# Kernel tuning notes

Measured on AMD Instinct MI355X. Metric: run time of the kernel, lower is better.

## Reference

```python
import jax, jax.numpy as jnp
import numpy as np
from math import sqrt, log

N_PATCHES = 128
ATTN_WINDOW = 10
NEG_INF = -10000.0


def _causal_mask(L):
    # patch id per position; query patch i may attend key patch j iff 0 < (j_pid - i_pid) < window
    channels = L // N_PATCHES
    pid = jnp.repeat(jnp.arange(N_PATCHES), channels)  # [L]
    diff = pid[None, :] - pid[:, None]                 # [L_query, L_key] = pid[key]-pid[query]
    return (diff <= 0) | (diff >= ATTN_WINDOW)         # True => blocked


def setup_inputs() -> dict:
    key = jax.random.key(0)
    kq, kk, kv = jax.random.split(key, 3)
    B, H, L, D = 4, 8, 1024, 64
    return {
        "queries": jax.random.normal(kq, (B, H, L, D), dtype=jnp.float32),
        "keys": jax.random.normal(kk, (B, H, L, D), dtype=jnp.float32),
        "values": jax.random.normal(kv, (B, H, L, D), dtype=jnp.float32),
        "log_scale": jnp.asarray(np.log(2.0), dtype=jnp.float32),
    }


def reference(queries, keys, values, log_scale):
    B, H, L, D = queries.shape
    scores = jnp.einsum("bhld,bhmd->bhlm", queries, keys)           # [B,H,L,L]
    scale = jnp.clip(jnp.exp(log_scale), 1.0, 30.0) / sqrt(D)
    mask = _causal_mask(L)                                          # [L,L]
    pos = jnp.where(mask, NEG_INF, scores)
    neg = jnp.where(mask, NEG_INF, -scores)
    A = jax.nn.softmax(scale * pos, axis=-1) - jax.nn.softmax(scale * neg, axis=-1)
    V = jnp.einsum("bhlm,bhmd->bhld", A, values)
    return V
```

## Files before the change

kernel.cpp:

```cpp
#include <hip/hip_runtime.h>
#include <math.h>

#define NPATCH 128
#define CH 8
#define D 64
#define G 8
#define NQ (G*CH)
#define NKEY 128
#define KSTR 72
#define VSTR 136
#define PSTR 100

typedef __fp16 half8 __attribute__((ext_vector_type(8)));
typedef float  f32x4 __attribute__((ext_vector_type(4)));
typedef unsigned u32x4 __attribute__((ext_vector_type(4)));

static __device__ __forceinline__ unsigned pk(float x, float y) {
    return __builtin_bit_cast(unsigned, __builtin_amdgcn_cvt_pkrtz(x, y));
}
static __device__ __forceinline__ half8 ld8(const unsigned short* p) {
    return __builtin_bit_cast(half8, *(const u32x4*)p);
}
static __device__ __forceinline__ half8 mk8(const float4& a, const float4& b) {
    u32x4 u = { pk(a.x, a.y), pk(a.z, a.w), pk(b.x, b.y), pk(b.z, b.w) };
    return __builtin_bit_cast(half8, u);
}

__global__ __launch_bounds__(256) void signed_attn_kernel(
    const float* __restrict__ Q, const float* __restrict__ K,
    const float* __restrict__ V, const float* __restrict__ logscale,
    float* __restrict__ O)
{
    __shared__ __align__(16) unsigned short sK[NKEY * KSTR];
    __shared__ __align__(16) unsigned short sVt[D * VSTR];
    __shared__ __align__(16) unsigned short sP[NQ * PSTR];

    const int tid = threadIdx.x;
    const int grp = blockIdx.x & 15;
    const int bh  = blockIdx.x >> 4;
    const int p0  = grp * G;

    const long long base = (long long)bh * (NPATCH * CH) * D;
    const int nst = min(NKEY, (NPATCH - 1 - p0) * CH);

    const float scale = fminf(fmaxf(__expf(logscale[0]), 1.0f), 30.0f) * 0.125f;

    {
        const float4* Kg = (const float4*)(K + base + (long long)((p0 + 1) * CH) * D);
        for (int i = tid; i < NKEY * 16; i += 256) {
            const int row = i >> 4, d4 = i & 15;
            uint2 w = make_uint2(0u, 0u);
            if (row < nst) { const float4 v = Kg[i]; w = make_uint2(pk(v.x, v.y), pk(v.z, v.w)); }
            *(uint2*)&sK[row * KSTR + d4 * 4] = w;
        }
        const float4* Vg = (const float4*)(V + base + (long long)((p0 + 1) * CH) * D);
        for (int u = tid; u < 64 * 16; u += 256) {
            const int kp = u & 63, dq = u >> 6;
            float4 va = make_float4(0.f, 0.f, 0.f, 0.f);
            float4 vb = va;
            if (2 * kp < nst) { va = Vg[(2 * kp) * 16 + dq]; vb = Vg[(2 * kp + 1) * 16 + dq]; }
            *(unsigned*)&sVt[(dq * 4 + 0) * VSTR + 2 * kp] = pk(va.x, vb.x);
            *(unsigned*)&sVt[(dq * 4 + 1) * VSTR + 2 * kp] = pk(va.y, vb.y);
            *(unsigned*)&sVt[(dq * 4 + 2) * VSTR + 2 * kp] = pk(va.z, vb.z);
            *(unsigned*)&sVt[(dq * 4 + 3) * VSTR + 2 * kp] = pk(va.w, vb.w);
        }
    }

    const int wav = tid >> 6, lane = tid & 63;
    const int col = lane & 15, quad = lane >> 4;

    const float4* Qg4 = (const float4*)(Q + base + (long long)(p0 * CH + wav * 16 + col) * D);
    const half8 a0 = mk8(Qg4[quad * 2],     Qg4[quad * 2 + 1]);
    const half8 a1 = mk8(Qg4[8 + quad * 2], Qg4[9 + quad * 2]);

    __syncthreads();

    f32x4 acc[5];
#pragma unroll
    for (int t = 0; t < 5; ++t) acc[t] = (f32x4){0.f, 0.f, 0.f, 0.f};
#pragma unroll
    for (int t = 0; t < 5; ++t) {
        const int krow = (wav + t) * 16 + col;
        const half8 b0 = ld8(&sK[krow * KSTR + quad * 8]);
        const half8 b1 = ld8(&sK[krow * KSTR + 32 + quad * 8]);
        acc[t] = __builtin_amdgcn_mfma_f32_16x16x32_f16(a0, b0, acc[t], 0, 0, 0);
        acc[t] = __builtin_amdgcn_mfma_f32_16x16x32_f16(a1, b1, acc[t], 0, 0, 0);
    }

#pragma unroll
    for (int r = 0; r < 4; ++r) {
        const int q   = wav * 16 + quad * 4 + r;
        const int kr0 = (q >> 3) * 8;
        const int kmx = min(kr0 + 72, nst);

        float tv[5]; bool vl[5];
        float mp = -1e30f, mn = -1e30f;
#pragma unroll
        for (int t = 0; t < 5; ++t) {
            const int c = (wav + t) * 16 + col;
            tv[t] = scale * acc[t][r];
            vl[t] = (c >= kr0) && (c < kmx);
            mp = fmaxf(mp, vl[t] ?  tv[t] : -1e30f);
            mn = fmaxf(mn, vl[t] ? -tv[t] : -1e30f);
        }
#pragma unroll
        for (int off = 1; off < 16; off <<= 1) {
            mp = fmaxf(mp, __shfl_xor(mp, off));
            mn = fmaxf(mn, __shfl_xor(mn, off));
        }
        float ep[5], en[5], sp = 0.f, sn = 0.f;
#pragma unroll
        for (int t = 0; t < 5; ++t) {
            ep[t] = vl[t] ? __expf( tv[t] - mp) : 0.f;
            en[t] = vl[t] ? __expf(-tv[t] - mn) : 0.f;
            sp += ep[t]; sn += en[t];
        }
#pragma unroll
        for (int off = 1; off < 16; off <<= 1) {
            sp += __shfl_xor(sp, off);
            sn += __shfl_xor(sn, off);
        }
        const float rp = (sp > 0.f) ? 1.f / sp : 0.f;
        const float rn = (sn > 0.f) ? 1.f / sn : 0.f;
#pragma unroll
        for (int t = 0; t < 5; ++t) {
            const float A = ep[t] * rp - en[t] * rn;
            sP[q * PSTR + t * 16 + col] = (unsigned short)pk(A, A);
        }
        sP[q * PSTR + 80 + col] = 0;
    }

    f32x4 oc[4];
#pragma unroll
    for (int t = 0; t < 4; ++t) oc[t] = (f32x4){0.f, 0.f, 0.f, 0.f};
#pragma unroll
    for (int kq = 0; kq < 3; ++kq) {
        const half8 ap = ld8(&sP[(wav * 16 + col) * PSTR + kq * 32 + quad * 8]);
        const int kb = wav * 16 + kq * 32 + quad * 8;
        const int kcl = (kb <= 120) ? kb : 120;
#pragma unroll
        for (int t = 0; t < 4; ++t) {
            const half8 bv = ld8(&sVt[(t * 16 + col) * VSTR + kcl]);
            oc[t] = __builtin_amdgcn_mfma_f32_16x16x32_f16(ap, bv, oc[t], 0, 0, 0);
        }
    }

    float* Ob = O + base + (long long)(p0 * CH) * D;
#pragma unroll
    for (int t = 0; t < 4; ++t) {
#pragma unroll
        for (int r = 0; r < 4; ++r) {
            Ob[(wav * 16 + quad * 4 + r) * D + t * 16 + col] = oc[t][r];
        }
    }
}

extern "C" void kernel_launch(void* const* d_in, const int* in_sizes, int n_in,
                              void* d_out, int out_size, void* d_ws, size_t ws_size,
                              hipStream_t stream) {
    const float* Q  = (const float*)d_in[0];
    const float* K  = (const float*)d_in[1];
    const float* V  = (const float*)d_in[2];
    const float* ls = (const float*)d_in[3];
    float* O = (float*)d_out;

    const int L = 1024;
    const int nBH = in_sizes[0] / (L * D);
    dim3 grid(nBH * (NPATCH / G));
    signed_attn_kernel<<<grid, 256, 0, stream>>>(Q, K, V, ls, O);
}
```

Before: 82.50 us.

## Defer V transpose to after softmax and pack softmax reductions into fp16 pairs

All global loads (Q, V, K) are issued up front. V is held in registers and written transposed to shared memory only after the QK and softmax phase, with an extra barrier before the PV MFMA. This is meant to overlap V load latency with compute. The softmax max and sum cross-lane reductions now pack the positive and negative branches into one fp16x2 shuffle, halving shuffle count. The cost is higher register pressure from holding 32 floats of V per thread, and lower precision: fp16 sums and maxes risk accuracy loss or overflow.

```diff
diff --git a/kernel.cpp b/kernel.cpp
--- a/kernel.cpp
+++ b/kernel.cpp
@@ -12,11 +12,21 @@
 #define PSTR 100
 
 typedef __fp16 half8 __attribute__((ext_vector_type(8)));
+typedef __fp16 h2    __attribute__((ext_vector_type(2)));
 typedef float  f32x4 __attribute__((ext_vector_type(4)));
 typedef unsigned u32x4 __attribute__((ext_vector_type(4)));
 
 static __device__ __forceinline__ unsigned pk(float x, float y) {
     return __builtin_bit_cast(unsigned, __builtin_amdgcn_cvt_pkrtz(x, y));
+}
+static __device__ __forceinline__ h2 pk2(float x, float y) {
+    return __builtin_amdgcn_cvt_pkrtz(x, y);
+}
+static __device__ __forceinline__ h2 pkmax(h2 a, h2 b) {
+    h2 r; r[0] = a[0] > b[0] ? a[0] : b[0]; r[1] = a[1] > b[1] ? a[1] : b[1]; return r;
+}
+static __device__ __forceinline__ h2 shfl_h2(h2 v, int off) {
+    return __builtin_bit_cast(h2, __shfl_xor(__builtin_bit_cast(int, v), off));
 }
 static __device__ __forceinline__ half8 ld8(const unsigned short* p) {
     return __builtin_bit_cast(half8, *(const u32x4*)p);
@@ -45,35 +55,40 @@
 
     const float scale = fminf(fmaxf(__expf(logscale[0]), 1.0f), 30.0f) * 0.125f;
 
+    const int wav = tid >> 6, lane = tid & 63;
+    const int col = lane & 15, quad = lane >> 4;
+
+    const float4* Qg4 = (const float4*)(Q + base + (long long)(p0 * CH + wav * 16 + col) * D);
+    const float4 q00 = Qg4[quad * 2],     q01 = Qg4[quad * 2 + 1];
+    const float4 q10 = Qg4[8 + quad * 2], q11 = Qg4[9 + quad * 2];
+
+    const float4* Vg = (const float4*)(V + base + (long long)((p0 + 1) * CH) * D);
+    float4 va[4], vb[4];
+#pragma unroll
+    for (int it = 0; it < 4; ++it) {
+        const int u = tid + it * 256;
+        const int kp = u & 63;
+        va[it] = make_float4(0.f, 0.f, 0.f, 0.f);
+        vb[it] = va[it];
+        if (2 * kp < nst) { va[it] = Vg[(2 * kp) * 16 + (u >> 6)];
+                            vb[it] = Vg[(2 * kp + 1) * 16 + (u >> 6)]; }
+    }
+
     {
         const float4* Kg = (const float4*)(K + base + (long long)((p0 + 1) * CH) * D);
-        for (int i = tid; i < NKEY * 16; i += 256) {
+#pragma unroll
+        for (int it = 0; it < 8; ++it) {
+            const int i = tid + it * 256;
             const int row = i >> 4, d4 = i & 15;
             uint2 w = make_uint2(0u, 0u);
             if (row < nst) { const float4 v = Kg[i]; w = make_uint2(pk(v.x, v.y), pk(v.z, v.w)); }
             *(uint2*)&sK[row * KSTR + d4 * 4] = w;
         }
-        const float4* Vg = (const float4*)(V + base + (long long)((p0 + 1) * CH) * D);
-        for (int u = tid; u < 64 * 16; u += 256) {
-            const int kp = u & 63, dq = u >> 6;
-            float4 va = make_float4(0.f, 0.f, 0.f, 0.f);
-            float4 vb = va;
-            if (2 * kp < nst) { va = Vg[(2 * kp) * 16 + dq]; vb = Vg[(2 * kp + 1) * 16 + dq]; }
-            *(unsigned*)&sVt[(dq * 4 + 0) * VSTR + 2 * kp] = pk(va.x, vb.x);
-            *(unsigned*)&sVt[(dq * 4 + 1) * VSTR + 2 * kp] = pk(va.y, vb.y);
-            *(unsigned*)&sVt[(dq * 4 + 2) * VSTR + 2 * kp] = pk(va.z, vb.z);
-            *(unsigned*)&sVt[(dq * 4 + 3) * VSTR + 2 * kp] = pk(va.w, vb.w);
-        }
     }
+    __syncthreads();
 
-    const int wav = tid >> 6, lane = tid & 63;
-    const int col = lane & 15, quad = lane >> 4;
-
-    const float4* Qg4 = (const float4*)(Q + base + (long long)(p0 * CH + wav * 16 + col) * D);
-    const half8 a0 = mk8(Qg4[quad * 2],     Qg4[quad * 2 + 1]);
-    const half8 a1 = mk8(Qg4[8 + quad * 2], Qg4[9 + quad * 2]);
-
-    __syncthreads();
+    const half8 a0 = mk8(q00, q01);
+    const half8 a1 = mk8(q10, q11);
 
     f32x4 acc[5];
 #pragma unroll
@@ -94,32 +109,31 @@
         const int kmx = min(kr0 + 72, nst);
 
         float tv[5]; bool vl[5];
-        float mp = -1e30f, mn = -1e30f;
+        float mpl = -1e30f, mnl = -1e30f;
 #pragma unroll
         for (int t = 0; t < 5; ++t) {
             const int c = (wav + t) * 16 + col;
             tv[t] = scale * acc[t][r];
             vl[t] = (c >= kr0) && (c < kmx);
-            mp = fmaxf(mp, vl[t] ?  tv[t] : -1e30f);
-            mn = fmaxf(mn, vl[t] ? -tv[t] : -1e30f);
+            mpl = fmaxf(mpl, vl[t] ?  tv[t] : -1e30f);
+            mnl = fmaxf(mnl, vl[t] ? -tv[t] : -1e30f);
         }
+        h2 pm = pk2(mpl, mnl);
 #pragma unroll
-        for (int off = 1; off < 16; off <<= 1) {
-            mp = fmaxf(mp, __shfl_xor(mp, off));
-            mn = fmaxf(mn, __shfl_xor(mn, off));
-        }
-        float ep[5], en[5], sp = 0.f, sn = 0.f;
+        for (int off = 1; off < 16; off <<= 1) pm = pkmax(pm, shfl_h2(pm, off));
+        const float mp = (float)pm[0], mn = (float)pm[1];
+
+        float ep[5], en[5], spl = 0.f, snl = 0.f;
 #pragma unroll
         for (int t = 0; t < 5; ++t) {
             ep[t] = vl[t] ? __expf( tv[t] - mp) : 0.f;
             en[t] = vl[t] ? __expf(-tv[t] - mn) : 0.f;
-            sp += ep[t]; sn += en[t];
+            spl += ep[t]; snl += en[t];
         }
+        h2 ss = pk2(spl, snl);
 #pragma unroll
-        for (int off = 1; off < 16; off <<= 1) {
-            sp += __shfl_xor(sp, off);
-            sn += __shfl_xor(sn, off);
-        }
+        for (int off = 1; off < 16; off <<= 1) ss = ss + shfl_h2(ss, off);
+        const float sp = (float)ss[0], sn = (float)ss[1];
         const float rp = (sp > 0.f) ? 1.f / sp : 0.f;
         const float rn = (sn > 0.f) ? 1.f / sn : 0.f;
 #pragma unroll
@@ -129,6 +143,17 @@
         }
         sP[q * PSTR + 80 + col] = 0;
     }
+
+#pragma unroll
+    for (int it = 0; it < 4; ++it) {
+        const int u = tid + it * 256;
+        const int kp = u & 63, dq = u >> 6;
+        *(unsigned*)&sVt[(dq * 4 + 0) * VSTR + 2 * kp] = pk(va[it].x, vb[it].x);
+        *(unsigned*)&sVt[(dq * 4 + 1) * VSTR + 2 * kp] = pk(va[it].y, vb[it].y);
+        *(unsigned*)&sVt[(dq * 4 + 2) * VSTR + 2 * kp] = pk(va[it].z, vb[it].z);
+        *(unsigned*)&sVt[(dq * 4 + 3) * VSTR + 2 * kp] = pk(va[it].w, vb[it].w);
+    }
+    __syncthreads();
 
     f32x4 oc[4];
 #pragma unroll
```

Result: slower. 85.79 us (+4.0%).

## Load K fragments directly into registers, skip LDS staging, defer barrier

Applied to the files above, without the earlier changes.

K is no longer staged through shared memory. Each lane loads its MFMA B-fragment rows of K straight from global memory into registers and converts them to fp16 in place. The barrier moves to just before the P·V stage, so the QK MFMAs and the softmax run while the V transpose into LDS completes. This removes the LDS writes and reads for K and an early synchronisation point. In exchange it costs more registers, and K rows are read redundantly across waves because windows overlap, which adds global or L2 traffic.

```diff
diff --git a/kernel.cpp b/kernel.cpp
--- a/kernel.cpp
+++ b/kernel.cpp
@@ -7,7 +7,6 @@
 #define G 8
 #define NQ (G*CH)
 #define NKEY 128
-#define KSTR 72
 #define VSTR 136
 #define PSTR 100
 
@@ -31,7 +30,6 @@
     const float* __restrict__ V, const float* __restrict__ logscale,
     float* __restrict__ O)
 {
-    __shared__ __align__(16) unsigned short sK[NKEY * KSTR];
     __shared__ __align__(16) unsigned short sVt[D * VSTR];
     __shared__ __align__(16) unsigned short sP[NQ * PSTR];
 
@@ -45,16 +43,29 @@
 
     const float scale = fminf(fmaxf(__expf(logscale[0]), 1.0f), 30.0f) * 0.125f;
 
+    const int wav = tid >> 6, lane = tid & 63;
+    const int col = lane & 15, quad = lane >> 4;
+
+    const float4* Qg4 = (const float4*)(Q + base + (long long)(p0 * CH + wav * 16 + col) * D);
+    const float4 q00 = Qg4[quad * 2],     q01 = Qg4[quad * 2 + 1];
+    const float4 q10 = Qg4[8 + quad * 2], q11 = Qg4[9 + quad * 2];
+
+    const float4* Kg4 = (const float4*)(K + base + (long long)((p0 + 1) * CH) * D);
+    float4 kf[5][4];
+#pragma unroll
+    for (int t = 0; t < 5; ++t) {
+        const int krel = (wav + t) * 16 + col;
+        const int kcl  = (krel < nst) ? krel : (nst - 1);
+        const float4* Kr = Kg4 + kcl * 16;
+        kf[t][0] = Kr[quad * 2];     kf[t][1] = Kr[quad * 2 + 1];
+        kf[t][2] = Kr[8 + quad * 2]; kf[t][3] = Kr[9 + quad * 2];
+    }
+
     {
-        const float4* Kg = (const float4*)(K + base + (long long)((p0 + 1) * CH) * D);
-        for (int i = tid; i < NKEY * 16; i += 256) {
-            const int row = i >> 4, d4 = i & 15;
-            uint2 w = make_uint2(0u, 0u);
-            if (row < nst) { const float4 v = Kg[i]; w = make_uint2(pk(v.x, v.y), pk(v.z, v.w)); }
-            *(uint2*)&sK[row * KSTR + d4 * 4] = w;
-        }
         const float4* Vg = (const float4*)(V + base + (long long)((p0 + 1) * CH) * D);
-        for (int u = tid; u < 64 * 16; u += 256) {
+#pragma unroll
+        for (int it = 0; it < 4; ++it) {
+            const int u = tid + it * 256;
             const int kp = u & 63, dq = u >> 6;
             float4 va = make_float4(0.f, 0.f, 0.f, 0.f);
             float4 vb = va;
@@ -66,23 +77,16 @@
         }
     }
 
-    const int wav = tid >> 6, lane = tid & 63;
-    const int col = lane & 15, quad = lane >> 4;
-
-    const float4* Qg4 = (const float4*)(Q + base + (long long)(p0 * CH + wav * 16 + col) * D);
-    const half8 a0 = mk8(Qg4[quad * 2],     Qg4[quad * 2 + 1]);
-    const half8 a1 = mk8(Qg4[8 + quad * 2], Qg4[9 + quad * 2]);
-
-    __syncthreads();
+    const half8 a0 = mk8(q00, q01);
+    const half8 a1 = mk8(q10, q11);
 
     f32x4 acc[5];
 #pragma unroll
     for (int t = 0; t < 5; ++t) acc[t] = (f32x4){0.f, 0.f, 0.f, 0.f};
 #pragma unroll
     for (int t = 0; t < 5; ++t) {
-        const int krow = (wav + t) * 16 + col;
-        const half8 b0 = ld8(&sK[krow * KSTR + quad * 8]);
-        const half8 b1 = ld8(&sK[krow * KSTR + 32 + quad * 8]);
+        const half8 b0 = mk8(kf[t][0], kf[t][1]);
+        const half8 b1 = mk8(kf[t][2], kf[t][3]);
         acc[t] = __builtin_amdgcn_mfma_f32_16x16x32_f16(a0, b0, acc[t], 0, 0, 0);
         acc[t] = __builtin_amdgcn_mfma_f32_16x16x32_f16(a1, b1, acc[t], 0, 0, 0);
     }
@@ -130,6 +134,8 @@
         sP[q * PSTR + 80 + col] = 0;
     }
 
+    __syncthreads();
+
     f32x4 oc[4];
 #pragma unroll
     for (int t = 0; t < 4; ++t) oc[t] = (f32x4){0.f, 0.f, 0.f, 0.f};
```

After: 85.14 us. +3.2%, slower.
